# Performance work log

Measured on AMD Instinct MI355X. Metric: run time of the kernel, lower is better.

The kernel has to match this reference:

```python
import jax, jax.numpy as jnp
from jax import lax
import numpy as np

# dims
VOCAB = 64
B, L = 64, 2048
EMB = 128
D_MODEL = 128
N_LAYERS = 4
D_INNER = 256      # expand=2
D_STATE = 16
D_CONV = 4
DT_RANK = 8        # ceil(d_model/16)
NCLS = 3
BN_EPS = 1e-5
RMS_EPS = 1e-5


def setup_inputs():
    key = jax.random.key(0)
    ks = iter(jax.random.split(key, 48))
    def rn(shape, s=0.02):
        return jax.random.normal(next(ks), shape, jnp.float32) * s
    tokens = jax.random.randint(next(ks), (B, L), 0, VOCAB)
    mask = jnp.ones((B, L), jnp.float32)
    emb = rn((VOCAB, EMB)).at[0].set(0.0)  # padding_idx=0
    bn_w = jnp.ones((EMB,), jnp.float32)
    bn_b = jnp.zeros((EMB,), jnp.float32)
    conv_w = rn((D_MODEL, EMB, 3))
    conv_b = jnp.zeros((D_MODEL,), jnp.float32)
    in_proj_w = rn((N_LAYERS, 2 * D_INNER, D_MODEL))
    conv1d_w = rn((N_LAYERS, D_INNER, D_CONV), 0.1)
    conv1d_b = jnp.zeros((N_LAYERS, D_INNER), jnp.float32)
    x_proj_w = rn((N_LAYERS, DT_RANK + 2 * D_STATE, D_INNER))
    dt_proj_w = rn((N_LAYERS, D_INNER, DT_RANK), 0.1)
    dt_proj_b = rn((N_LAYERS, D_INNER), 0.1)
    A_log = jnp.tile(jnp.log(jnp.arange(1, D_STATE + 1, dtype=jnp.float32))[None, None, :],
                     (N_LAYERS, D_INNER, 1))
    D_param = jnp.ones((N_LAYERS, D_INNER), jnp.float32)
    out_proj_w = rn((N_LAYERS, D_MODEL, D_INNER))
    norm_w = jnp.ones((N_LAYERS, D_MODEL), jnp.float32)
    lin1_w = rn((512, D_MODEL)); lin1_b = jnp.zeros((512,), jnp.float32)
    lin2_w = rn((512, 512));     lin2_b = jnp.zeros((512,), jnp.float32)
    lin3_w = rn((NCLS, 512));    lin3_b = jnp.zeros((NCLS,), jnp.float32)
    return dict(tokens=tokens, mask=mask, emb=emb, bn_w=bn_w, bn_b=bn_b,
                conv_w=conv_w, conv_b=conv_b, in_proj_w=in_proj_w,
                conv1d_w=conv1d_w, conv1d_b=conv1d_b, x_proj_w=x_proj_w,
                dt_proj_w=dt_proj_w, dt_proj_b=dt_proj_b, A_log=A_log,
                D_param=D_param, out_proj_w=out_proj_w, norm_w=norm_w,
                lin1_w=lin1_w, lin1_b=lin1_b, lin2_w=lin2_w, lin2_b=lin2_b,
                lin3_w=lin3_w, lin3_b=lin3_b)


def _rmsnorm(x, w):
    return x * lax.rsqrt(jnp.mean(x * x, axis=-1, keepdims=True) + RMS_EPS) * w


def _selective_scan(u, dt, A, Bm, Cm, Dv):
    # u, dt: (B,L,di); A: (di,ds); Bm, Cm: (B,L,ds); Dv: (di,)
    def step(h, inp):
        dt_t, B_t, C_t, u_t = inp           # (B,di),(B,ds),(B,ds),(B,di)
        dA = jnp.exp(dt_t[:, :, None] * A)  # (B,di,ds)
        h = dA * h + (dt_t * u_t)[:, :, None] * B_t[:, None, :]
        y = jnp.einsum('bds,bs->bd', h, C_t)
        return h, y
    h0 = jnp.zeros((u.shape[0], A.shape[0], A.shape[1]), u.dtype)
    xs = (jnp.swapaxes(dt, 0, 1), jnp.swapaxes(Bm, 0, 1),
          jnp.swapaxes(Cm, 0, 1), jnp.swapaxes(u, 0, 1))
    _, ys = lax.scan(step, h0, xs)          # ys: (L,B,di)
    return jnp.swapaxes(ys, 0, 1) + u * Dv


def _mamba(x, in_w, cw, cb, xp_w, dtp_w, dtp_b, A_log, Dv, out_w):
    # x: (B,L,d_model)
    xz = jnp.einsum('bld,ed->ble', x, in_w)            # (B,L,2*di)
    xi, z = jnp.split(xz, 2, axis=-1)
    # causal depthwise conv over time
    xc = jnp.swapaxes(xi, 1, 2)                        # (B,di,L)
    xc = lax.conv_general_dilated(xc, cw[:, None, :], (1,), [(D_CONV - 1, 0)],
                                  dimension_numbers=('NCH', 'OIH', 'NCH'),
                                  feature_group_count=D_INNER)
    xc = jax.nn.silu(xc + cb[None, :, None])
    xc = jnp.swapaxes(xc, 1, 2)                        # (B,L,di)
    x_dbl = jnp.einsum('bld,ed->ble', xc, xp_w)        # (B,L,dtr+2*ds)
    dt = jax.nn.softplus(jnp.einsum('blr,dr->bld', x_dbl[..., :DT_RANK], dtp_w) + dtp_b)
    Bm = x_dbl[..., DT_RANK:DT_RANK + D_STATE]
    Cm = x_dbl[..., DT_RANK + D_STATE:]
    A = -jnp.exp(A_log)                                # (di,ds)
    y = _selective_scan(xc, dt, A, Bm, Cm, Dv)
    y = y * jax.nn.silu(z)
    return jnp.einsum('ble,de->bld', y, out_w)         # (B,L,d_model)


def _forward(tokens, mask, emb, bn_w, bn_b, conv_w, conv_b, in_proj_w,
             conv1d_w, conv1d_b, x_proj_w, dt_proj_w, dt_proj_b, A_log,
             D_param, out_proj_w, norm_w, lin1_w, lin1_b, lin2_w, lin2_b,
             lin3_w, lin3_b):
    x = emb[tokens]                                    # (B,L,E)
    xc = jnp.swapaxes(x, 1, 2)                         # (B,E,L)
    # BatchNorm1d in eval mode: running_mean=0, running_var=1
    xc = xc * (bn_w * lax.rsqrt(jnp.array(1.0 + BN_EPS)))[None, :, None] + bn_b[None, :, None]
    xc = lax.conv_general_dilated(xc, conv_w, (1,), [(1, 1)],
                                  dimension_numbers=('NCH', 'OIH', 'NCH'))
    xc = jax.nn.relu(xc + conv_b[None, :, None])
    x = jnp.swapaxes(xc, 1, 2)                         # (B,L,D_MODEL)
    for i in range(N_LAYERS):
        x = _mamba(_rmsnorm(x, norm_w[i]), in_proj_w[i], conv1d_w[i],
                   conv1d_b[i], x_proj_w[i], dt_proj_w[i], dt_proj_b[i],
                   A_log[i], D_param[i], out_proj_w[i]) + x
    # masked average pooling
    m = mask[:, :, None]
    denom = jnp.clip(jnp.sum(m, axis=1), 1e-9, None)   # (B,1)->(B,D) broadcast
    pooled = jnp.sum(x * m, axis=1) / denom
    h = jax.nn.relu(pooled @ lin1_w.T + lin1_b)
    h = jax.nn.relu(h @ lin2_w.T + lin2_b)
    return h @ lin3_w.T + lin3_b                       # (B,NCLS)


def reference(tokens, mask, emb, bn_w, bn_b, conv_w, conv_b, in_proj_w,
              conv1d_w, conv1d_b, x_proj_w, dt_proj_w, dt_proj_b, A_log,
              D_param, out_proj_w, norm_w, lin1_w, lin1_b, lin2_w, lin2_b,
              lin3_w, lin3_b):
    return _forward(tokens, mask, emb, bn_w, bn_b, conv_w, conv_b, in_proj_w,
                    conv1d_w, conv1d_b, x_proj_w, dt_proj_w, dt_proj_b, A_log,
                    D_param, out_proj_w, norm_w, lin1_w, lin1_b, lin2_w,
                    lin2_b, lin3_w, lin3_b)
```

## Files before the change

### kernel.cpp

```cpp
#include <hip/hip_runtime.h>
#include <math.h>

#define NB     64
#define SL     2048
#define NTOK   (NB*SL)
#define EMB_D  128
#define DMODEL 128
#define DIN    256
#define DST    16
#define NLAYER 4
#define SEG    64
#define NSEG   (SL/SEG)
#define L2E    1.4426950408889634f
#define LN2    0.6931471805599453f

typedef __bf16 bf16x8 __attribute__((ext_vector_type(8)));
typedef __bf16 bf16x4 __attribute__((ext_vector_type(4)));
typedef float  f32x4  __attribute__((ext_vector_type(4)));

#define FIX_PL   ((size_t)0)
#define FIX_PM   (FIX_PL + 131072)
#define FIX_PD   (FIX_PM + 1024)
#define FIX_H1   (FIX_PD + 8192)
#define FIX_H2   (FIX_H1 + 32768)
#define FIX_WP   (FIX_H2 + 32768)
#define FIX_W2B  (FIX_WP + 65536)
#define FIX_WINB (FIX_W2B + 24576)
#define FIX_WOUTB (FIX_WINB + 131072)
#define FIX_END  (FIX_WOUTB + 65536)

__device__ __forceinline__ float fexp2(float x){ return __builtin_amdgcn_exp2f(x); }
__device__ __forceinline__ float flog2(float x){ return __builtin_amdgcn_logf(x); }
__device__ __forceinline__ float frcp (float x){ return __builtin_amdgcn_rcpf(x); }
__device__ __forceinline__ float fast_exp(float x){ return fexp2(x*L2E); }
__device__ __forceinline__ float siluf(float v){ return v * frcp(1.f + fast_exp(-v)); }
__device__ __forceinline__ float softplusf(float a){
  return fmaxf(a,0.f) + flog2(1.f + fexp2(-fabsf(a)*L2E)) * LN2;
}
__device__ __forceinline__ unsigned short bfbits(float x){
  __bf16 b = (__bf16)x; return __builtin_bit_cast(unsigned short, b);
}
__device__ __forceinline__ unsigned int packdu(float dt, float u){
  return ((unsigned int)bfbits(u) << 16) | (unsigned int)bfbits(dt);
}

#define SPSA(hA,hB,q,s0,s1) { float eA=fexp2(dt*(-fast_exp(alog[d*DST+s0])*L2E)); \
                              hA=fmaf(eA,hA,du*q.x); \
                              float eB=fexp2(dt*(-fast_exp(alog[d*DST+s1])*L2E)); \
                              hB=fmaf(eB,hB,du*q.z); }
#define SPSY(hA,hB,q,s0,s1) { float eA=fexp2(dt*(-fast_exp(alog[d*DST+s0])*L2E)); \
                              hA=fmaf(eA,hA,du*q.x); y=fmaf(hA,q.y,y); \
                              float eB=fexp2(dt*(-fast_exp(alog[d*DST+s1])*L2E)); \
                              hB=fmaf(eB,hB,du*q.z); y=fmaf(hB,q.w,y); }

#define POWTREE(r) \
  float r2=(r)*(r), r4=r2*r2, r8=r4*r4; \
  float r3=r2*(r), r5=r4*(r), r6=r4*r2, r7=r4*r3; \
  float r9=r8*(r), r10=r8*r2, r11=r8*r3, r12=r8*r4; \
  float r13=r8*r5, r14=r8*r6, r15=r8*r7, r16=r8*r8;

__global__ void k_w2b(const float* __restrict__ cw, __bf16* __restrict__ w2){
  int g = blockIdx.x*256 + threadIdx.x;
  if (g >= 128*384) return;
  int d = g / 384, j = g % 384;
  int k = j >> 7, e = j & 127;
  w2[d*384 + k*128 + e] = (__bf16)cw[d*384 + e*3 + k];
}

__global__ void k_cvt(const float* __restrict__ src, __bf16* __restrict__ dst, int n){
  int i = blockIdx.x*256 + threadIdx.x;
  if (i < n) dst[i] = (__bf16)src[i];
}

__global__ void k_wprep(const float* __restrict__ xpw, __bf16* __restrict__ wp){
  int g = blockIdx.x*256 + threadIdx.x;
  int l = g >> 14, rem = g & 16383;
  int n = rem >> 8, k = rem & 255;
  float v = 0.f;
  if (n < 8){
    v = xpw[(size_t)l*40*256 + n*256 + k];
  } else if (n < 40){
    int i = n - 8;
    int row = 8 + ((i&1)<<4) + (i>>1);
    v = xpw[(size_t)l*40*256 + row*256 + k];
  }
  wp[g] = (__bf16)v;
}

__global__ void k_embed(const int* __restrict__ tok, const float* __restrict__ emb,
                        const float* __restrict__ bnw, const float* __restrict__ bnb,
                        float* __restrict__ xp){
  int r = blockIdx.x;
  int e = threadIdx.x;
  int b = r / 2050, tp = r % 2050;
  float v = 0.f;
  if (tp != 0 && tp != 2049){
    int t = tp - 1;
    int id = tok[(size_t)b*SL + t];
    float s = bnw[e] * rsqrtf(1.0f + 1e-5f);
    v = emb[(size_t)id*EMB_D + e] * s + bnb[e];
  }
  xp[(size_t)r*EMB_D + e] = v;
}

__global__ __launch_bounds__(256) void k_rmsscale(const float* __restrict__ x,
                                                  float* __restrict__ rs){
  int wv = threadIdx.x>>6, lane = threadIdx.x&63;
  size_t tok = (size_t)blockIdx.x*4 + wv;
  float2 v = *(const float2*)(x + tok*128 + lane*2);
  float ss = v.x*v.x + v.y*v.y;
  #pragma unroll
  for (int m=1;m<64;m<<=1) ss += __shfl_xor(ss, m);
  float r = rsqrtf(ss*(1.f/128.f) + 1e-5f);
  if (lane == 0) rs[tok] = r;
}

template<int MODE, int K, int N>
__global__ __launch_bounds__(256) void k_mgemm(
    const void* __restrict__ Av, const __bf16* __restrict__ Wb,
    const float* __restrict__ bias, const float* __restrict__ rsp,
    const float* __restrict__ nwp,
    float* __restrict__ out, __bf16* __restrict__ outb, __bf16* __restrict__ outz){
  __shared__ __bf16 As[128][40];
  __shared__ __bf16 Bs[128][40];
  const int tid  = threadIdx.x;
  const int wave = tid >> 6;
  const int lane = tid & 63;
  const int col  = lane & 15;
  const int quad = lane >> 4;
  const int wm = (wave & 1) * 64;
  const int wn = (wave >> 1) * 64;
  const int m0 = blockIdx.y * 128;
  const int n0 = blockIdx.x * 128;

  f32x4 acc[4][4];
  #pragma unroll
  for (int i=0;i<4;i++)
    #pragma unroll
    for (int j=0;j<4;j++) acc[i][j] = (f32x4){0.f,0.f,0.f,0.f};

  size_t abase;
  if constexpr(MODE==0){
    int bb = m0 >> 11, tloc = m0 & 2047;
    abase = ((size_t)bb*2050 + tloc) * 128;
  } else {
    abase = (size_t)m0 * K;
  }

  const int sm = tid >> 3;
  const int sk4 = (tid & 7) * 4;
  const int bn = tid >> 2;
  const int bk8 = (tid & 3) * 8;

  for (int k0 = 0; k0 < K; k0 += 32){
    #pragma unroll
    for (int p=0;p<4;p++){
      int m = p*32 + sm;
      const float* A = (const float*)Av;
      float4 v;
      if constexpr(MODE==0){
        v = *(const float4*)(A + abase + (size_t)m*128 + k0 + sk4);
      } else {
        float4 x4 = *(const float4*)(A + abase + (size_t)m*K + k0 + sk4);
        float4 w4 = *(const float4*)(nwp + k0 + sk4);
        float s = rsp[m0 + m];
        v.x = x4.x*s*w4.x; v.y = x4.y*s*w4.y; v.z = x4.z*s*w4.z; v.w = x4.w*s*w4.w;
      }
      bf16x4 o;
      o[0] = (__bf16)v.x; o[1] = (__bf16)v.y; o[2] = (__bf16)v.z; o[3] = (__bf16)v.w;
      *(bf16x4*)&As[m][sk4] = o;
    }
    #pragma unroll
    for (int p=0;p<2;p++){
      int n = p*64 + bn;
      bf16x8 w = *(const bf16x8*)(Wb + (size_t)(n0+n)*K + k0 + bk8);
      *(bf16x8*)&Bs[n][bk8] = w;
    }
    __syncthreads();
    bf16x8 af[4], bfr[4];
    const int fq = quad*8;
    #pragma unroll
    for (int i=0;i<4;i++) af[i]  = *(const bf16x8*)&As[wm + i*16 + col][fq];
    #pragma unroll
    for (int j=0;j<4;j++) bfr[j] = *(const bf16x8*)&Bs[wn + j*16 + col][fq];
    #pragma unroll
    for (int i=0;i<4;i++)
      #pragma unroll
      for (int j=0;j<4;j++)
        acc[i][j] = __builtin_amdgcn_mfma_f32_16x16x32_bf16(af[i], bfr[j], acc[i][j], 0, 0, 0);
    __syncthreads();
  }

  #pragma unroll
  for (int i=0;i<4;i++){
    #pragma unroll
    for (int j=0;j<4;j++){
      int n_l = wn + j*16 + col;
      #pragma unroll
      for (int r=0;r<4;r++){
        int m = m0 + wm + i*16 + quad*4 + r;
        float c = acc[i][j][r];
        if constexpr(MODE==0){
          int n = n0 + n_l;
          out[(size_t)m*DMODEL + n] = fmaxf(c + bias[n], 0.f);
        } else {
          int n = n0 + n_l;
          if (n < DIN) outb[(size_t)m*DIN + n]        = (__bf16)c;
          else         outz[(size_t)m*DIN + n - DIN]  = (__bf16)siluf(c);
        }
      }
    }
  }
}

__global__ __launch_bounds__(256) void k_seg(const __bf16* __restrict__ xi,
    const __bf16* __restrict__ wpb,
    const float* __restrict__ cw, const float* __restrict__ cb,
    const float* __restrict__ dtw, const float* __restrict__ dtb,
    const float* __restrict__ alog,
    float* __restrict__ vbc, unsigned int* __restrict__ dub,
    float* __restrict__ cseg, float* __restrict__ sdtb){
  __shared__ __bf16 sxc[64][264];
  __shared__ float vls[64][68];
  const int tid = threadIdx.x;
  const size_t m0 = (size_t)blockIdx.x * 64;
  const int b = (int)(m0 >> 11);
  const int g = (int)((m0 >> 6) & (NSEG-1));
  const int seq0 = (int)(m0 & 2047);

  {
    const int c4 = (tid & 63) * 4;
    const int tw = tid >> 6;
    float wc[4][4];
    #pragma unroll
    for (int j=0;j<4;j++)
      #pragma unroll
      for (int k=0;k<4;k++) wc[j][k] = cw[(c4+j)*4 + k];
    float4 cb4 = *(const float4*)(cb + c4);
    #pragma unroll
    for (int it=0; it<16; it++){
      int t = it*4 + tw;
      float4 acc = cb4;
      #pragma unroll
      for (int k=0;k<4;k++){
        if (seq0 + t - 3 + k >= 0){
          bf16x4 xv = *(const bf16x4*)(xi + (m0 + t - 3 + k)*DIN + c4);
          acc.x = fmaf(wc[0][k], (float)xv[0], acc.x);
          acc.y = fmaf(wc[1][k], (float)xv[1], acc.y);
          acc.z = fmaf(wc[2][k], (float)xv[2], acc.z);
          acc.w = fmaf(wc[3][k], (float)xv[3], acc.w);
        }
      }
      bf16x4 o;
      o[0]=(__bf16)siluf(acc.x); o[1]=(__bf16)siluf(acc.y);
      o[2]=(__bf16)siluf(acc.z); o[3]=(__bf16)siluf(acc.w);
      *(bf16x4*)&sxc[t][c4] = o;
    }
  }
  __syncthreads();

  {
    const int wave = tid >> 6, lane = tid & 63;
    const int col = lane & 15, quad = lane >> 4;
    const int wn = wave * 16;
    f32x4 acc[4];
    #pragma unroll
    for (int i=0;i<4;i++) acc[i] = (f32x4){0.f,0.f,0.f,0.f};
    #pragma unroll
    for (int kc=0;kc<8;kc++){
      bf16x8 bfr = *(const bf16x8*)(wpb + (size_t)(wn+col)*256 + kc*32 + quad*8);
      #pragma unroll
      for (int mi=0;mi<4;mi++){
        bf16x8 af = *(const bf16x8*)&sxc[mi*16 + col][kc*32 + quad*8];
        acc[mi] = __builtin_amdgcn_mfma_f32_16x16x32_bf16(af, bfr, acc[mi], 0, 0, 0);
      }
    }
    #pragma unroll
    for (int mi=0;mi<4;mi++)
      #pragma unroll
      for (int r=0;r<4;r++)
        vls[mi*16 + quad*4 + r][wn + col] = acc[mi][r];
  }
  __syncthreads();

  #pragma unroll
  for (int p=0;p<8;p++){
    int j = p*256 + tid;
    int t = j >> 5, i = j & 31;
    vbc[(m0+t)*32 + i] = vls[t][8+i];
  }

  {
    const int d = tid;
    const float a0 = -fast_exp(alog[d*DST]) * L2E;
    bool fast = true;
    for (int s=1;s<16;s++){
      float as = -fast_exp(alog[d*DST + s]) * L2E;
      fast = fast && (fabsf(as - (float)(s+1)*a0) <= 1e-3f*fabsf(as));
    }
    float4 w8a = *(const float4*)(dtw + d*8);
    float4 w8b = *(const float4*)(dtw + d*8 + 4);
    const float bd = dtb[d];
    float h0=0.f,h1=0.f,h2=0.f,h3=0.f,h4=0.f,h5=0.f,h6=0.f,h7=0.f;
    float h8=0.f,h9=0.f,h10=0.f,h11=0.f,h12=0.f,h13=0.f,h14=0.f,h15=0.f;
    float ssum = 0.f;
    if (fast){
      for (int t=0;t<SEG;t++){
        float4 v0 = *(const float4*)&vls[t][0];
        float4 v1 = *(const float4*)&vls[t][4];
        float lin = bd;
        lin = fmaf(v0.x,w8a.x, fmaf(v0.y,w8a.y, fmaf(v0.z,w8a.z, fmaf(v0.w,w8a.w, lin))));
        lin = fmaf(v1.x,w8b.x, fmaf(v1.y,w8b.y, fmaf(v1.z,w8b.z, fmaf(v1.w,w8b.w, lin))));
        float dt = softplusf(lin);
        ssum += dt;
        float u = (float)sxc[t][d];
        dub[(m0+t)*DIN + d] = packdu(dt, u);
        float du = dt*u;
        float r1 = fexp2(dt*a0);
        POWTREE(r1)
        float4 q0 = *(const float4*)&vls[t][8];
        float4 q1 = *(const float4*)&vls[t][12];
        float4 q2 = *(const float4*)&vls[t][16];
        float4 q3 = *(const float4*)&vls[t][20];
        float4 q4 = *(const float4*)&vls[t][24];
        float4 q5 = *(const float4*)&vls[t][28];
        float4 q6 = *(const float4*)&vls[t][32];
        float4 q7 = *(const float4*)&vls[t][36];
        h0 =fmaf(r1 ,h0 ,du*q0.x); h1 =fmaf(r2 ,h1 ,du*q0.z);
        h2 =fmaf(r3 ,h2 ,du*q1.x); h3 =fmaf(r4 ,h3 ,du*q1.z);
        h4 =fmaf(r5 ,h4 ,du*q2.x); h5 =fmaf(r6 ,h5 ,du*q2.z);
        h6 =fmaf(r7 ,h6 ,du*q3.x); h7 =fmaf(r8 ,h7 ,du*q3.z);
        h8 =fmaf(r9 ,h8 ,du*q4.x); h9 =fmaf(r10,h9 ,du*q4.z);
        h10=fmaf(r11,h10,du*q5.x); h11=fmaf(r12,h11,du*q5.z);
        h12=fmaf(r13,h12,du*q6.x); h13=fmaf(r14,h13,du*q6.z);
        h14=fmaf(r15,h14,du*q7.x); h15=fmaf(r16,h15,du*q7.z);
      }
    } else {
      for (int t=0;t<SEG;t++){
        float4 v0 = *(const float4*)&vls[t][0];
        float4 v1 = *(const float4*)&vls[t][4];
        float lin = bd;
        lin = fmaf(v0.x,w8a.x, fmaf(v0.y,w8a.y, fmaf(v0.z,w8a.z, fmaf(v0.w,w8a.w, lin))));
        lin = fmaf(v1.x,w8b.x, fmaf(v1.y,w8b.y, fmaf(v1.z,w8b.z, fmaf(v1.w,w8b.w, lin))));
        float dt = softplusf(lin);
        ssum += dt;
        float u = (float)sxc[t][d];
        dub[(m0+t)*DIN + d] = packdu(dt, u);
        float du = dt*u;
        float4 q0 = *(const float4*)&vls[t][8];
        float4 q1 = *(const float4*)&vls[t][12];
        float4 q2 = *(const float4*)&vls[t][16];
        float4 q3 = *(const float4*)&vls[t][20];
        float4 q4 = *(const float4*)&vls[t][24];
        float4 q5 = *(const float4*)&vls[t][28];
        float4 q6 = *(const float4*)&vls[t][32];
        float4 q7 = *(const float4*)&vls[t][36];
        SPSA(h0,h1,q0,0,1)   SPSA(h2,h3,q1,2,3)   SPSA(h4,h5,q2,4,5)   SPSA(h6,h7,q3,6,7)
        SPSA(h8,h9,q4,8,9)   SPSA(h10,h11,q5,10,11) SPSA(h12,h13,q6,12,13) SPSA(h14,h15,q7,14,15)
      }
    }
    size_t base = (((size_t)b*NSEG + g)*DIN + d)*DST;
    float4 o;
    o.x=h0; o.y=h1; o.z=h2; o.w=h3;     *(float4*)(cseg + base     ) = o;
    o.x=h4; o.y=h5; o.z=h6; o.w=h7;     *(float4*)(cseg + base +  4) = o;
    o.x=h8; o.y=h9; o.z=h10; o.w=h11;   *(float4*)(cseg + base +  8) = o;
    o.x=h12; o.y=h13; o.z=h14; o.w=h15; *(float4*)(cseg + base + 12) = o;
    sdtb[((size_t)b*NSEG + g)*DIN + d] = ssum;
  }
}

__global__ __launch_bounds__(256) void k_scanB(float* __restrict__ cseg,
    const float* __restrict__ sdtb, const float* __restrict__ alog){
  int gl = blockIdx.x*256 + threadIdx.x;
  int b   = gl >> 12;
  int rem = gl & 4095;
  int d = rem >> 4, s = rem & 15;
  const float a = -fast_exp(alog[d*DST + s]) * L2E;
  float h = 0.f;
  for (int g=0; g<NSEG; g++){
    size_t base = ((size_t)b*NSEG + g)*DIN;
    float sd = sdtb[base + d];
    size_t ci = (base + d)*DST + s;
    float c = cseg[ci];
    cseg[ci] = h;
    h = fmaf(fexp2(a*sd), h, c);
  }
}

__global__ __launch_bounds__(256) void k_scanC3(float* __restrict__ xres,
    const unsigned int* __restrict__ dub, const float* __restrict__ vbc,
    const __bf16* __restrict__ gzb,
    const float* __restrict__ alog, const float* __restrict__ Dpar,
    const float* __restrict__ cseg, const __bf16* __restrict__ wout,
    float* __restrict__ rs){
  __shared__ __bf16 sy[64][264];
  __shared__ float svbc[64][32];
  float* sx = (float*)sy;
  const int tid = threadIdx.x;
  const size_t m0 = (size_t)blockIdx.x * 64;
  const int b = (int)(m0 >> 11);
  const int g = (int)((m0 >> 6) & (NSEG-1));

  #pragma unroll
  for (int p=0;p<8;p++){
    int j = p*256 + tid;
    int t = j >> 5, i = j & 31;
    svbc[t][i] = vbc[(m0+t)*32 + i];
  }

  {
    const int d = tid;
    const float a0 = -fast_exp(alog[d*DST]) * L2E;
    bool fast = true;
    for (int s=1;s<16;s++){
      float as = -fast_exp(alog[d*DST + s]) * L2E;
      fast = fast && (fabsf(as - (float)(s+1)*a0) <= 1e-3f*fabsf(as));
    }
    const float Dv = Dpar[d];
    size_t base = (((size_t)b*NSEG + g)*DIN + d)*DST;
    float4 hv0 = *(const float4*)(cseg + base);
    float4 hv1 = *(const float4*)(cseg + base + 4);
    float4 hv2 = *(const float4*)(cseg + base + 8);
    float4 hv3 = *(const float4*)(cseg + base + 12);
    float h0=hv0.x,h1=hv0.y,h2=hv0.z,h3=hv0.w;
    float h4=hv1.x,h5=hv1.y,h6=hv1.z,h7=hv1.w;
    float h8=hv2.x,h9=hv2.y,h10=hv2.z,h11=hv2.w;
    float h12=hv3.x,h13=hv3.y,h14=hv3.z,h15=hv3.w;
    __syncthreads();

    if (fast){
      for (int t=0;t<SEG;t++){
        unsigned int w = dub[(m0+t)*DIN + d];
        float u  = __builtin_bit_cast(float, w & 0xffff0000u);
        float dt = __builtin_bit_cast(float, w << 16);
        float du = dt*u;
        float r1 = fexp2(dt*a0);
        POWTREE(r1)
        float4 q0 = *(const float4*)&svbc[t][0];
        float4 q1 = *(const float4*)&svbc[t][4];
        float4 q2 = *(const float4*)&svbc[t][8];
        float4 q3 = *(const float4*)&svbc[t][12];
        float4 q4 = *(const float4*)&svbc[t][16];
        float4 q5 = *(const float4*)&svbc[t][20];
        float4 q6 = *(const float4*)&svbc[t][24];
        float4 q7 = *(const float4*)&svbc[t][28];
        h0 =fmaf(r1 ,h0 ,du*q0.x); h1 =fmaf(r2 ,h1 ,du*q0.z);
        h2 =fmaf(r3 ,h2 ,du*q1.x); h3 =fmaf(r4 ,h3 ,du*q1.z);
        h4 =fmaf(r5 ,h4 ,du*q2.x); h5 =fmaf(r6 ,h5 ,du*q2.z);
        h6 =fmaf(r7 ,h6 ,du*q3.x); h7 =fmaf(r8 ,h7 ,du*q3.z);
        h8 =fmaf(r9 ,h8 ,du*q4.x); h9 =fmaf(r10,h9 ,du*q4.z);
        h10=fmaf(r11,h10,du*q5.x); h11=fmaf(r12,h11,du*q5.z);
        h12=fmaf(r13,h12,du*q6.x); h13=fmaf(r14,h13,du*q6.z);
        h14=fmaf(r15,h14,du*q7.x); h15=fmaf(r16,h15,du*q7.z);
        float ya = fmaf(h0,q0.y, fmaf(h1,q0.w, fmaf(h2,q1.y, h3*q1.w)));
        float yb = fmaf(h4,q2.y, fmaf(h5,q2.w, fmaf(h6,q3.y, h7*q3.w)));
        float yc = fmaf(h8,q4.y, fmaf(h9,q4.w, fmaf(h10,q5.y, h11*q5.w)));
        float yd = fmaf(h12,q6.y, fmaf(h13,q6.w, fmaf(h14,q7.y, h15*q7.w)));
        float y = (ya+yb)+(yc+yd);
        float gz = (float)gzb[(m0+t)*DIN + d];
        sy[t][d] = (__bf16)((y + u*Dv) * gz);
      }
    } else {
      for (int t=0;t<SEG;t++){
        unsigned int w = dub[(m0+t)*DIN + d];
        float u  = __builtin_bit_cast(float, w & 0xffff0000u);
        float dt = __builtin_bit_cast(float, w << 16);
        float du = dt*u;
        float y = 0.f;
        float4 q0 = *(const float4*)&svbc[t][0];
        float4 q1 = *(const float4*)&svbc[t][4];
        float4 q2 = *(const float4*)&svbc[t][8];
        float4 q3 = *(const float4*)&svbc[t][12];
        float4 q4 = *(const float4*)&svbc[t][16];
        float4 q5 = *(const float4*)&svbc[t][20];
        float4 q6 = *(const float4*)&svbc[t][24];
        float4 q7 = *(const float4*)&svbc[t][28];
        SPSY(h0,h1,q0,0,1)   SPSY(h2,h3,q1,2,3)   SPSY(h4,h5,q2,4,5)   SPSY(h6,h7,q3,6,7)
        SPSY(h8,h9,q4,8,9)   SPSY(h10,h11,q5,10,11) SPSY(h12,h13,q6,12,13) SPSY(h14,h15,q7,14,15)
        float gz = (float)gzb[(m0+t)*DIN + d];
        sy[t][d] = (__bf16)((y + u*Dv) * gz);
      }
    }
  }
  __syncthreads();

  const int wave = tid >> 6, lane = tid & 63;
  const int col = lane & 15, quad = lane >> 4;
  const int wn = wave * 32;
  f32x4 acc[4][2];
  #pragma unroll
  for (int i=0;i<4;i++)
    #pragma unroll
    for (int j=0;j<2;j++) acc[i][j] = (f32x4){0.f,0.f,0.f,0.f};
  #pragma unroll
  for (int kc=0;kc<8;kc++){
    bf16x8 bfr0 = *(const bf16x8*)(wout + (size_t)(wn +      col)*256 + kc*32 + quad*8);
    bf16x8 bfr1 = *(const bf16x8*)(wout + (size_t)(wn + 16 + col)*256 + kc*32 + quad*8);
    #pragma unroll
    for (int mi=0;mi<4;mi++){
      bf16x8 af = *(const bf16x8*)&sy[mi*16 + col][kc*32 + quad*8];
      acc[mi][0] = __builtin_amdgcn_mfma_f32_16x16x32_bf16(af, bfr0, acc[mi][0], 0, 0, 0);
      acc[mi][1] = __builtin_amdgcn_mfma_f32_16x16x32_bf16(af, bfr1, acc[mi][1], 0, 0, 0);
    }
  }
  __syncthreads();

  #pragma unroll
  for (int mi=0;mi<4;mi++){
    #pragma unroll
    for (int j=0;j<2;j++){
      int n = wn + j*16 + col;
      #pragma unroll
      for (int r=0;r<4;r++){
        int ml = mi*16 + quad*4 + r;
        size_t go = (m0 + ml)*DMODEL + n;
        float nx = xres[go] + acc[mi][j][r];
        xres[go] = nx;
        sx[ml*132 + n] = nx;
      }
    }
  }
  __syncthreads();
  {
    int row = tid >> 2, q = tid & 3;
    const float* pr = sx + row*132 + q*32;
    float ss = 0.f;
    #pragma unroll
    for (int i=0;i<32;i+=4){
      float4 v = *(const float4*)(pr + i);
      ss += v.x*v.x + v.y*v.y + v.z*v.z + v.w*v.w;
    }
    ss += __shfl_xor(ss, 1);
    ss += __shfl_xor(ss, 2);
    if (q == 0) rs[m0 + row] = rsqrtf(ss*(1.f/128.f) + 1e-5f);
  }
}

__global__ __launch_bounds__(256) void k_pool1(const float* __restrict__ x,
    const float* __restrict__ mask, float* __restrict__ part, float* __restrict__ pmask){
  int b = blockIdx.y, seg = blockIdx.x;
  int d = threadIdx.x & 127, half = threadIdx.x >> 7;
  int t0 = seg*128 + half*64;
  float acc = 0.f, macc = 0.f;
  for (int i=0;i<64;i++){
    int t = t0 + i;
    float mv = mask[(size_t)b*SL + t];
    acc = fmaf(x[((size_t)b*SL + t)*DMODEL + d], mv, acc);
    macc += mv;
  }
  __shared__ float sm[256];
  __shared__ float smm[2];
  sm[threadIdx.x] = acc;
  if (d == 0) smm[half] = macc;
  __syncthreads();
  if (half == 0){
    part[((size_t)b*16 + seg)*128 + d] = sm[d] + sm[128+d];
    if (d == 0) pmask[b*16 + seg] = smm[0] + smm[1];
  }
}

__global__ void k_pool2(const float* __restrict__ part, const float* __restrict__ pmask,
                        float* __restrict__ pooled){
  int b = blockIdx.x, d = threadIdx.x;
  float acc = 0.f, ms = 0.f;
  for (int s=0;s<16;s++){ acc += part[((size_t)b*16+s)*128 + d]; ms += pmask[b*16+s]; }
  pooled[(size_t)b*128 + d] = acc / fmaxf(ms, 1e-9f);
}

__global__ void k_mlp_a(const float* __restrict__ in, const float* __restrict__ w,
                        const float* __restrict__ bias, float* __restrict__ out, int K){
  int b = blockIdx.y;
  int n = blockIdx.x*128 + threadIdx.x;
  const float4* pw = (const float4*)(w + (size_t)n*K);
  const float4* pi = (const float4*)(in + (size_t)b*K);
  float acc = 0.f;
  for (int k=0;k<K/4;k++){
    float4 a = pi[k], ww = pw[k];
    acc = fmaf(a.x,ww.x, fmaf(a.y,ww.y, fmaf(a.z,ww.z, fmaf(a.w,ww.w, acc))));
  }
  out[(size_t)b*512 + n] = fmaxf(acc + bias[n], 0.f);
}

__global__ void k_mlp3(const float* __restrict__ h, const float* __restrict__ w,
                       const float* __restrict__ bias, float* __restrict__ out){
  int b = blockIdx.x;
  int n = threadIdx.x >> 6, lane = threadIdx.x & 63;
  if (n >= 3) return;
  float acc = 0.f;
  for (int k=lane; k<512; k+=64) acc = fmaf(h[(size_t)b*512+k], w[(size_t)n*512+k], acc);
  #pragma unroll
  for (int m=1;m<64;m<<=1) acc += __shfl_xor(acc, m);
  if (lane == 0) out[(size_t)b*3 + n] = acc + bias[n];
}

extern "C" void kernel_launch(void* const* d_in, const int* in_sizes, int n_in,
                              void* d_out, int out_size, void* d_ws, size_t ws_size,
                              hipStream_t stream){
  const int*   tokens = (const int*)  d_in[0];
  const float* mask   = (const float*)d_in[1];
  const float* emb    = (const float*)d_in[2];
  const float* bn_w   = (const float*)d_in[3];
  const float* bn_b   = (const float*)d_in[4];
  const float* conv_w = (const float*)d_in[5];
  const float* conv_b = (const float*)d_in[6];
  const float* in_w   = (const float*)d_in[7];
  const float* c1_w   = (const float*)d_in[8];
  const float* c1_b   = (const float*)d_in[9];
  const float* xp_w   = (const float*)d_in[10];
  const float* dtp_w  = (const float*)d_in[11];
  const float* dtp_b  = (const float*)d_in[12];
  const float* A_log  = (const float*)d_in[13];
  const float* D_par  = (const float*)d_in[14];
  const float* out_w  = (const float*)d_in[15];
  const float* nrm_w  = (const float*)d_in[16];
  const float* l1w = (const float*)d_in[17]; const float* l1b = (const float*)d_in[18];
  const float* l2w = (const float*)d_in[19]; const float* l2b = (const float*)d_in[20];
  const float* l3w = (const float*)d_in[21]; const float* l3b = (const float*)d_in[22];
  float* dout = (float*)d_out;

  int CB = 64;
  while (CB > 1 && ((size_t)CB*SL*741 + FIX_END)*4 > ws_size) CB >>= 1;
  if (((size_t)CB*SL*741 + FIX_END)*4 > ws_size) return;
  const size_t CTOK = (size_t)CB*SL;

  float* ws  = (float*)d_ws;
  float* pl  = ws + FIX_PL;
  float* pm  = ws + FIX_PM;
  float* pd  = ws + FIX_PD;
  float* h1  = ws + FIX_H1;
  float* h2  = ws + FIX_H2;
  __bf16* wpb   = (__bf16*)(ws + FIX_WP);
  __bf16* w2b   = (__bf16*)(ws + FIX_W2B);
  __bf16* winb  = (__bf16*)(ws + FIX_WINB);
  __bf16* woutb = (__bf16*)(ws + FIX_WOUTB);
  float* xcb = ws + FIX_END;
  float* rs  = xcb + CTOK*128;
  __bf16* xib = (__bf16*)(rs + CTOK);
  unsigned int* dub = (unsigned int*)(xib + CTOK*256);
  float* pad = (float*)xib;
  float* vbc = (float*)(dub + CTOK*256);
  float* csg = vbc + CTOK*32;
  float* sdt = csg + CTOK*64;
  __bf16* zb  = (__bf16*)(sdt + CTOK*4);

  k_w2b<<<192, 256, 0, stream>>>(conv_w, w2b);
  k_cvt<<<1024, 256, 0, stream>>>(in_w,  winb,  4*512*128);
  k_cvt<<<512,  256, 0, stream>>>(out_w, woutb, 4*128*256);
  k_wprep<<<256, 256, 0, stream>>>(xp_w, wpb);

  const int nchunks = NB / CB;
  for (int c = 0; c < nchunks; c++){
    const int* tok_c = tokens + (size_t)c*CTOK;

    k_embed<<<CB*2050, 128, 0, stream>>>(tok_c, emb, bn_w, bn_b, pad);
    k_mgemm<0,384,128><<<dim3(1, CTOK/128), 256, 0, stream>>>(
        pad, w2b, conv_b, nullptr, nullptr, xcb, nullptr, nullptr);
    k_rmsscale<<<CTOK/4, 256, 0, stream>>>(xcb, rs);

    for (int layer = 0; layer < NLAYER; layer++){
      const __bf16* lin = winb  + (size_t)layer*512*128;
      const float* lcw  = c1_w  + (size_t)layer*DIN*4;
      const float* lcb  = c1_b  + (size_t)layer*DIN;
      const float* ldw  = dtp_w + (size_t)layer*DIN*8;
      const float* ldb  = dtp_b + (size_t)layer*DIN;
      const float* lal  = A_log + (size_t)layer*DIN*DST;
      const float* lD   = D_par + (size_t)layer*DIN;
      const __bf16* low = woutb + (size_t)layer*128*256;
      const float* lnw  = nrm_w + (size_t)layer*128;

      k_mgemm<1,128,512><<<dim3(4, CTOK/128), 256, 0, stream>>>(
          xcb, lin, nullptr, rs, lnw, nullptr, xib, zb);
      k_seg<<<(int)(CTOK/64), 256, 0, stream>>>(
          xib, wpb + (size_t)layer*64*256, lcw, lcb, ldw, ldb, lal, vbc, dub, csg, sdt);
      k_scanB<<<CB*16, 256, 0, stream>>>(csg, sdt, lal);
      k_scanC3<<<(int)(CTOK/64), 256, 0, stream>>>(
          xcb, dub, vbc, zb, lal, lD, csg, low, rs);
    }

    k_pool1<<<dim3(16, CB), 256, 0, stream>>>(
        xcb, mask + (size_t)c*CTOK, pl + (size_t)c*CB*16*128, pm + (size_t)c*CB*16);
  }

  k_pool2<<<NB, 128, 0, stream>>>(pl, pm, pd);
  k_mlp_a<<<dim3(4, NB), 128, 0, stream>>>(pd, l1w, l1b, h1, 128);
  k_mlp_a<<<dim3(4, NB), 128, 0, stream>>>(h1, l2w, l2b, h2, 512);
  k_mlp3<<<NB, 256, 0, stream>>>(h2, l3w, l3b, dout);
}
```

Before: 1.588 ms.

## Compute local scan output in segment pass and apply carried state by decay

The segment kernel now computes the intra-segment output (including the D skip term) from a zero initial state and stores it packed with the running cumulative dt (bf16 output, fp16 cumsum) instead of storing dt and u. The final scan kernel no longer re-runs the recurrence. It adds the contribution of the incoming segment state decayed by exp(A·cumsum), which removes the second sequential 16-state recurrence per token. In exchange, the local output is rounded to bf16 before the carry is added and the cumulative dt is held at fp16 precision, which may hurt accuracy.

```diff
diff --git a/kernel.cpp b/kernel.cpp
--- a/kernel.cpp
+++ b/kernel.cpp
@@ -40,24 +40,22 @@
 __device__ __forceinline__ unsigned short bfbits(float x){
   __bf16 b = (__bf16)x; return __builtin_bit_cast(unsigned short, b);
 }
-__device__ __forceinline__ unsigned int packdu(float dt, float u){
-  return ((unsigned int)bfbits(u) << 16) | (unsigned int)bfbits(dt);
-}
-
-#define SPSA(hA,hB,q,s0,s1) { float eA=fexp2(dt*(-fast_exp(alog[d*DST+s0])*L2E)); \
-                              hA=fmaf(eA,hA,du*q.x); \
-                              float eB=fexp2(dt*(-fast_exp(alog[d*DST+s1])*L2E)); \
-                              hB=fmaf(eB,hB,du*q.z); }
-#define SPSY(hA,hB,q,s0,s1) { float eA=fexp2(dt*(-fast_exp(alog[d*DST+s0])*L2E)); \
-                              hA=fmaf(eA,hA,du*q.x); y=fmaf(hA,q.y,y); \
-                              float eB=fexp2(dt*(-fast_exp(alog[d*DST+s1])*L2E)); \
-                              hB=fmaf(eB,hB,du*q.z); y=fmaf(hB,q.w,y); }
+__device__ __forceinline__ unsigned int packyc(float yl, float cum){
+  _Float16 hc = (_Float16)cum;
+  return ((unsigned int)bfbits(yl) << 16) |
+         (unsigned int)__builtin_bit_cast(unsigned short, hc);
+}
 
 #define POWTREE(r) \
   float r2=(r)*(r), r4=r2*r2, r8=r4*r4; \
   float r3=r2*(r), r5=r4*(r), r6=r4*r2, r7=r4*r3; \
   float r9=r8*(r), r10=r8*r2, r11=r8*r3, r12=r8*r4; \
   float r13=r8*r5, r14=r8*r6, r15=r8*r7, r16=r8*r8;
+
+#define SPSY(hA,hB,q,s0,s1) { float eA=fexp2(dt*(-fast_exp(alog[d*DST+s0])*L2E)); \
+                              hA=fmaf(eA,hA,du*q.x); y=fmaf(hA,q.y,y); \
+                              float eB=fexp2(dt*(-fast_exp(alog[d*DST+s1])*L2E)); \
+                              hB=fmaf(eB,hB,du*q.z); y=fmaf(hB,q.w,y); }
 
 __global__ void k_w2b(const float* __restrict__ cw, __bf16* __restrict__ w2){
   int g = blockIdx.x*256 + threadIdx.x;
@@ -217,8 +215,8 @@
     const __bf16* __restrict__ wpb,
     const float* __restrict__ cw, const float* __restrict__ cb,
     const float* __restrict__ dtw, const float* __restrict__ dtb,
-    const float* __restrict__ alog,
-    float* __restrict__ vbc, unsigned int* __restrict__ dub,
+    const float* __restrict__ alog, const float* __restrict__ Dpar,
+    float* __restrict__ vbc, unsigned int* __restrict__ pk,
     float* __restrict__ cseg, float* __restrict__ sdtb){
   __shared__ __bf16 sxc[64][264];
   __shared__ float vls[64][68];
@@ -301,9 +299,10 @@
     float4 w8a = *(const float4*)(dtw + d*8);
     float4 w8b = *(const float4*)(dtw + d*8 + 4);
     const float bd = dtb[d];
+    const float Dv = Dpar[d];
     float h0=0.f,h1=0.f,h2=0.f,h3=0.f,h4=0.f,h5=0.f,h6=0.f,h7=0.f;
     float h8=0.f,h9=0.f,h10=0.f,h11=0.f,h12=0.f,h13=0.f,h14=0.f,h15=0.f;
-    float ssum = 0.f;
+    float cum = 0.f;
     if (fast){
       for (int t=0;t<SEG;t++){
         float4 v0 = *(const float4*)&vls[t][0];
@@ -312,9 +311,8 @@
         lin = fmaf(v0.x,w8a.x, fmaf(v0.y,w8a.y, fmaf(v0.z,w8a.z, fmaf(v0.w,w8a.w, lin))));
         lin = fmaf(v1.x,w8b.x, fmaf(v1.y,w8b.y, fmaf(v1.z,w8b.z, fmaf(v1.w,w8b.w, lin))));
         float dt = softplusf(lin);
-        ssum += dt;
+        cum += dt;
         float u = (float)sxc[t][d];
-        dub[(m0+t)*DIN + d] = packdu(dt, u);
         float du = dt*u;
         float r1 = fexp2(dt*a0);
         POWTREE(r1)
@@ -334,6 +332,12 @@
         h10=fmaf(r11,h10,du*q5.x); h11=fmaf(r12,h11,du*q5.z);
         h12=fmaf(r13,h12,du*q6.x); h13=fmaf(r14,h13,du*q6.z);
         h14=fmaf(r15,h14,du*q7.x); h15=fmaf(r16,h15,du*q7.z);
+        float ya = fmaf(h0,q0.y, fmaf(h1,q0.w, fmaf(h2,q1.y, h3*q1.w)));
+        float yb = fmaf(h4,q2.y, fmaf(h5,q2.w, fmaf(h6,q3.y, h7*q3.w)));
+        float yc = fmaf(h8,q4.y, fmaf(h9,q4.w, fmaf(h10,q5.y, h11*q5.w)));
+        float yd = fmaf(h12,q6.y, fmaf(h13,q6.w, fmaf(h14,q7.y, h15*q7.w)));
+        float yl = (ya+yb)+(yc+yd) + u*Dv;
+        pk[(m0+t)*DIN + d] = packyc(yl, cum);
       }
     } else {
       for (int t=0;t<SEG;t++){
@@ -343,10 +347,10 @@
         lin = fmaf(v0.x,w8a.x, fmaf(v0.y,w8a.y, fmaf(v0.z,w8a.z, fmaf(v0.w,w8a.w, lin))));
         lin = fmaf(v1.x,w8b.x, fmaf(v1.y,w8b.y, fmaf(v1.z,w8b.z, fmaf(v1.w,w8b.w, lin))));
         float dt = softplusf(lin);
-        ssum += dt;
+        cum += dt;
         float u = (float)sxc[t][d];
-        dub[(m0+t)*DIN + d] = packdu(dt, u);
         float du = dt*u;
+        float y = 0.f;
         float4 q0 = *(const float4*)&vls[t][8];
         float4 q1 = *(const float4*)&vls[t][12];
         float4 q2 = *(const float4*)&vls[t][16];
@@ -355,8 +359,10 @@
         float4 q5 = *(const float4*)&vls[t][28];
         float4 q6 = *(const float4*)&vls[t][32];
         float4 q7 = *(const float4*)&vls[t][36];
-        SPSA(h0,h1,q0,0,1)   SPSA(h2,h3,q1,2,3)   SPSA(h4,h5,q2,4,5)   SPSA(h6,h7,q3,6,7)
-        SPSA(h8,h9,q4,8,9)   SPSA(h10,h11,q5,10,11) SPSA(h12,h13,q6,12,13) SPSA(h14,h15,q7,14,15)
+        SPSY(h0,h1,q0,0,1)   SPSY(h2,h3,q1,2,3)   SPSY(h4,h5,q2,4,5)   SPSY(h6,h7,q3,6,7)
+        SPSY(h8,h9,q4,8,9)   SPSY(h10,h11,q5,10,11) SPSY(h12,h13,q6,12,13) SPSY(h14,h15,q7,14,15)
+        float yl = y + u*Dv;
+        pk[(m0+t)*DIN + d] = packyc(yl, cum);
       }
     }
     size_t base = (((size_t)b*NSEG + g)*DIN + d)*DST;
@@ -365,7 +371,7 @@
     o.x=h4; o.y=h5; o.z=h6; o.w=h7;     *(float4*)(cseg + base +  4) = o;
     o.x=h8; o.y=h9; o.z=h10; o.w=h11;   *(float4*)(cseg + base +  8) = o;
     o.x=h12; o.y=h13; o.z=h14; o.w=h15; *(float4*)(cseg + base + 12) = o;
-    sdtb[((size_t)b*NSEG + g)*DIN + d] = ssum;
+    sdtb[((size_t)b*NSEG + g)*DIN + d] = cum;
   }
 }
 
@@ -388,9 +394,9 @@
 }
 
 __global__ __launch_bounds__(256) void k_scanC3(float* __restrict__ xres,
-    const unsigned int* __restrict__ dub, const float* __restrict__ vbc,
+    const unsigned int* __restrict__ pk, const float* __restrict__ vbc,
     const __bf16* __restrict__ gzb,
-    const float* __restrict__ alog, const float* __restrict__ Dpar,
+    const float* __restrict__ alog,
     const float* __restrict__ cseg, const __bf16* __restrict__ wout,
     float* __restrict__ rs){
   __shared__ __bf16 sy[64][264];
@@ -416,25 +422,24 @@
       float as = -fast_exp(alog[d*DST + s]) * L2E;
       fast = fast && (fabsf(as - (float)(s+1)*a0) <= 1e-3f*fabsf(as));
     }
-    const float Dv = Dpar[d];
     size_t base = (((size_t)b*NSEG + g)*DIN + d)*DST;
     float4 hv0 = *(const float4*)(cseg + base);
     float4 hv1 = *(const float4*)(cseg + base + 4);
     float4 hv2 = *(const float4*)(cseg + base + 8);
     float4 hv3 = *(const float4*)(cseg + base + 12);
-    float h0=hv0.x,h1=hv0.y,h2=hv0.z,h3=hv0.w;
-    float h4=hv1.x,h5=hv1.y,h6=hv1.z,h7=hv1.w;
-    float h8=hv2.x,h9=hv2.y,h10=hv2.z,h11=hv2.w;
-    float h12=hv3.x,h13=hv3.y,h14=hv3.z,h15=hv3.w;
+    const float h0=hv0.x,h1=hv0.y,h2=hv0.z,h3=hv0.w;
+    const float h4=hv1.x,h5=hv1.y,h6=hv1.z,h7=hv1.w;
+    const float h8=hv2.x,h9=hv2.y,h10=hv2.z,h11=hv2.w;
+    const float h12=hv3.x,h13=hv3.y,h14=hv3.z,h15=hv3.w;
     __syncthreads();
 
     if (fast){
+      #pragma unroll 4
       for (int t=0;t<SEG;t++){
-        unsigned int w = dub[(m0+t)*DIN + d];
-        float u  = __builtin_bit_cast(float, w & 0xffff0000u);
-        float dt = __builtin_bit_cast(float, w << 16);
-        float du = dt*u;
-        float r1 = fexp2(dt*a0);
+        unsigned int w = pk[(m0+t)*DIN + d];
+        float yl = __builtin_bit_cast(float, w & 0xffff0000u);
+        float cum = (float)__builtin_bit_cast(_Float16, (unsigned short)(w & 0xffffu));
+        float r1 = fexp2(cum*a0);
         POWTREE(r1)
         float4 q0 = *(const float4*)&svbc[t][0];
         float4 q1 = *(const float4*)&svbc[t][4];
@@ -444,41 +449,29 @@
         float4 q5 = *(const float4*)&svbc[t][20];
         float4 q6 = *(const float4*)&svbc[t][24];
         float4 q7 = *(const float4*)&svbc[t][28];
-        h0 =fmaf(r1 ,h0 ,du*q0.x); h1 =fmaf(r2 ,h1 ,du*q0.z);
-        h2 =fmaf(r3 ,h2 ,du*q1.x); h3 =fmaf(r4 ,h3 ,du*q1.z);
-        h4 =fmaf(r5 ,h4 ,du*q2.x); h5 =fmaf(r6 ,h5 ,du*q2.z);
-        h6 =fmaf(r7 ,h6 ,du*q3.x); h7 =fmaf(r8 ,h7 ,du*q3.z);
-        h8 =fmaf(r9 ,h8 ,du*q4.x); h9 =fmaf(r10,h9 ,du*q4.z);
-        h10=fmaf(r11,h10,du*q5.x); h11=fmaf(r12,h11,du*q5.z);
-        h12=fmaf(r13,h12,du*q6.x); h13=fmaf(r14,h13,du*q6.z);
-        h14=fmaf(r15,h14,du*q7.x); h15=fmaf(r16,h15,du*q7.z);
-        float ya = fmaf(h0,q0.y, fmaf(h1,q0.w, fmaf(h2,q1.y, h3*q1.w)));
-        float yb = fmaf(h4,q2.y, fmaf(h5,q2.w, fmaf(h6,q3.y, h7*q3.w)));
-        float yc = fmaf(h8,q4.y, fmaf(h9,q4.w, fmaf(h10,q5.y, h11*q5.w)));
-        float yd = fmaf(h12,q6.y, fmaf(h13,q6.w, fmaf(h14,q7.y, h15*q7.w)));
-        float y = (ya+yb)+(yc+yd);
+        float ya = fmaf(h0*r1, q0.y, fmaf(h1*r2, q0.w, fmaf(h2*r3, q1.y, (h3*r4)*q1.w)));
+        float yb = fmaf(h4*r5, q2.y, fmaf(h5*r6, q2.w, fmaf(h6*r7, q3.y, (h7*r8)*q3.w)));
+        float yc = fmaf(h8*r9, q4.y, fmaf(h9*r10, q4.w, fmaf(h10*r11, q5.y, (h11*r12)*q5.w)));
+        float yd = fmaf(h12*r13, q6.y, fmaf(h13*r14, q6.w, fmaf(h14*r15, q7.y, (h15*r16)*q7.w)));
+        float y = yl + (ya+yb)+(yc+yd);
         float gz = (float)gzb[(m0+t)*DIN + d];
-        sy[t][d] = (__bf16)((y + u*Dv) * gz);
+        sy[t][d] = (__bf16)(y * gz);
       }
     } else {
       for (int t=0;t<SEG;t++){
-        unsigned int w = dub[(m0+t)*DIN + d];
-        float u  = __builtin_bit_cast(float, w & 0xffff0000u);
-        float dt = __builtin_bit_cast(float, w << 16);
-        float du = dt*u;
-        float y = 0.f;
-        float4 q0 = *(const float4*)&svbc[t][0];
-        float4 q1 = *(const float4*)&svbc[t][4];
-        float4 q2 = *(const float4*)&svbc[t][8];
-        float4 q3 = *(const float4*)&svbc[t][12];
-        float4 q4 = *(const float4*)&svbc[t][16];
-        float4 q5 = *(const float4*)&svbc[t][20];
-        float4 q6 = *(const float4*)&svbc[t][24];
-        float4 q7 = *(const float4*)&svbc[t][28];
-        SPSY(h0,h1,q0,0,1)   SPSY(h2,h3,q1,2,3)   SPSY(h4,h5,q2,4,5)   SPSY(h6,h7,q3,6,7)
-        SPSY(h8,h9,q4,8,9)   SPSY(h10,h11,q5,10,11) SPSY(h12,h13,q6,12,13) SPSY(h14,h15,q7,14,15)
+        unsigned int w = pk[(m0+t)*DIN + d];
+        float yl = __builtin_bit_cast(float, w & 0xffff0000u);
+        float cum = (float)__builtin_bit_cast(_Float16, (unsigned short)(w & 0xffffu));
+        float hh[16] = {h0,h1,h2,h3,h4,h5,h6,h7,h8,h9,h10,h11,h12,h13,h14,h15};
+        float y = yl;
+        #pragma unroll
+        for (int s=0;s<16;s++){
+          float as = -fast_exp(alog[d*DST + s]) * L2E;
+          float C = svbc[t][2*s + 1];
+          y = fmaf(fexp2(cum*as)*hh[s], C, y);
+        }
         float gz = (float)gzb[(m0+t)*DIN + d];
-        sy[t][d] = (__bf16)((y + u*Dv) * gz);
+        sy[t][d] = (__bf16)(y * gz);
       }
     }
   }
@@ -636,9 +629,9 @@
   float* xcb = ws + FIX_END;
   float* rs  = xcb + CTOK*128;
   __bf16* xib = (__bf16*)(rs + CTOK);
-  unsigned int* dub = (unsigned int*)(xib + CTOK*256);
+  unsigned int* pkb = (unsigned int*)(xib + CTOK*256);
   float* pad = (float*)xib;
-  float* vbc = (float*)(dub + CTOK*256);
+  float* vbc = (float*)(pkb + CTOK*256);
   float* csg = vbc + CTOK*32;
   float* sdt = csg + CTOK*64;
   __bf16* zb  = (__bf16*)(sdt + CTOK*4);
@@ -671,10 +664,10 @@
       k_mgemm<1,128,512><<<dim3(4, CTOK/128), 256, 0, stream>>>(
           xcb, lin, nullptr, rs, lnw, nullptr, xib, zb);
       k_seg<<<(int)(CTOK/64), 256, 0, stream>>>(
-          xib, wpb + (size_t)layer*64*256, lcw, lcb, ldw, ldb, lal, vbc, dub, csg, sdt);
+          xib, wpb + (size_t)layer*64*256, lcw, lcb, ldw, ldb, lal, lD, vbc, pkb, csg, sdt);
       k_scanB<<<CB*16, 256, 0, stream>>>(csg, sdt, lal);
       k_scanC3<<<(int)(CTOK/64), 256, 0, stream>>>(
-          xcb, dub, vbc, zb, lal, lD, csg, low, rs);
+          xcb, pkb, vbc, zb, lal, csg, low, rs);
     }
 
     k_pool1<<<dim3(16, CB), 256, 0, stream>>>(
```

New measurement: 1.918 ms. 1.21x slower.
